# Optimization experiments

Measured on AMD Instinct MI355X. Metric: run time of the kernel, lower is better.

Reference implementation:

```python
import jax, jax.numpy as jnp
import numpy as np

B, S, H, I, NH, E = 16, 512, 1024, 4096, 16, 8
DH = H // NH
EPS = 1e-12


def layer_norm(x, g, b):
    mu = jnp.mean(x, axis=-1, keepdims=True)
    var = jnp.mean(jnp.square(x - mu), axis=-1, keepdims=True)
    return (x - mu) * jax.lax.rsqrt(var + EPS) * g + b


def setup_inputs() -> dict:
    key = jax.random.key(0)
    ks = jax.random.split(key, 16)
    s_h = 1.0 / np.sqrt(H)
    s_i = 1.0 / np.sqrt(I)
    return {
        "hidden_states": jax.random.normal(ks[0], (B, S, H), jnp.float32),
        "Wq": jax.random.normal(ks[1], (H, H), jnp.float32) * s_h,
        "bq": jnp.zeros((H,), jnp.float32),
        "Wk": jax.random.normal(ks[2], (H, H), jnp.float32) * s_h,
        "bk": jnp.zeros((H,), jnp.float32),
        "Wv": jax.random.normal(ks[3], (H, H), jnp.float32) * s_h,
        "bv": jnp.zeros((H,), jnp.float32),
        "Wo": jax.random.normal(ks[4], (H, H), jnp.float32) * s_h,
        "bo": jnp.zeros((H,), jnp.float32),
        "ln1_g": jnp.ones((H,), jnp.float32),
        "ln1_b": jnp.zeros((H,), jnp.float32),
        "ln2_g": jnp.ones((H,), jnp.float32),
        "ln2_b": jnp.zeros((H,), jnp.float32),
        "gate_W": jax.random.normal(ks[5], (H, E), jnp.float32) * s_h,
        "W_up": jax.random.normal(ks[6], (E, H, I), jnp.float32) * s_h,
        "b_up": jnp.zeros((E, I), jnp.float32),
        "W_down": jax.random.normal(ks[7], (E, I, H), jnp.float32) * s_i,
        "b_down": jnp.zeros((E, H), jnp.float32),
    }


def reference(hidden_states, Wq, bq, Wk, bk, Wv, bv, Wo, bo,
              ln1_g, ln1_b, ln2_g, ln2_b, gate_W, W_up, b_up, W_down, b_down):
    x = hidden_states
    # --- BERT self-attention ---
    q = (x @ Wq + bq).reshape(B, S, NH, DH)
    k = (x @ Wk + bk).reshape(B, S, NH, DH)
    v = (x @ Wv + bv).reshape(B, S, NH, DH)
    scores = jnp.einsum("bqhd,bkhd->bhqk", q, k) / np.sqrt(DH)
    probs = jax.nn.softmax(scores, axis=-1)
    ctx = jnp.einsum("bhqk,bkhd->bqhd", probs, v).reshape(B, S, H)
    # BertSelfOutput: dense + residual + LayerNorm
    attn_out = layer_norm(ctx @ Wo + bo + x, ln1_g, ln1_b)

    # --- feed_forward_chunk: pre-LN, MoE, residual (residual on attn_out) ---
    x_ln = layer_norm(attn_out, ln2_g, ln2_b)
    router_output = jnp.einsum("bsh,he->bse", x_ln, gate_W)
    router_logits = jnp.mean(router_output, axis=1)          # [B, E]
    choice = jnp.argmax(router_logits, axis=-1)              # softmax-argmax == logits-argmax

    # per-sample top-1 expert: gather each sample's expert weights, batched GEMM
    Wu = W_up[choice]                                        # [B, H, I]
    Wd = W_down[choice]                                      # [B, I, H]
    h = jax.nn.gelu(jnp.einsum("bsh,bhi->bsi", x_ln, Wu) + b_up[choice][:, None, :],
                    approximate=False)
    moe = jnp.einsum("bsi,bih->bsh", h, Wd) + b_down[choice][:, None, :]
    layer_output = moe + attn_out
    return (layer_output, router_logits)
```

## Files before the change

kernel.cpp:

```cpp
#include <hip/hip_runtime.h>


typedef __attribute__((ext_vector_type(4))) float f32x4;
typedef __attribute__((ext_vector_type(8))) short s8v;
typedef __attribute__((ext_vector_type(4))) short s4v;
typedef unsigned short u16;

#define DEV static __device__ __forceinline__

DEV u16 f2bf(float f){
  union { float f; unsigned u; } v; v.f = f;
  unsigned r = v.u + 0x7fffu + ((v.u >> 16) & 1u);
  return (u16)(r >> 16);
}

DEV f32x4 mfma16(s8v a, s8v b, f32x4 c){
  return __builtin_amdgcn_mfma_f32_16x16x32_bf16(a, b, c, 0, 0, 0);
}

DEV float wave_sum(float s){
#pragma unroll
  for (int o = 1; o < 64; o <<= 1) s += __shfl_xor(s, o);
  return s;
}

#define ASYNC_COPY16(g, l) \
  __builtin_amdgcn_global_load_lds((const __attribute__((address_space(1))) void*)(g), \
                                   (__attribute__((address_space(3))) void*)(l), 16, 0, 0)

__global__ __launch_bounds__(256) void cvt_bf16(const float* __restrict__ in,
                                                u16* __restrict__ out)
{
  const size_t i = ((size_t)blockIdx.x * 256 + threadIdx.x) * 8;
  f32x4 a = *(const f32x4*)&in[i];
  f32x4 b = *(const f32x4*)&in[i + 4];
  s8v o;
#pragma unroll
  for (int j = 0; j < 4; ++j){ o[j] = (short)f2bf(a[j]); o[4 + j] = (short)f2bf(b[j]); }
  *(s8v*)&out[i] = o;
}

__global__ __launch_bounds__(256) void transpose_w(const float* __restrict__ in,
                                                   u16* __restrict__ out, int R, int C)
{
  __shared__ float t[32][33];
  const size_t bs = (size_t)blockIdx.z * R * (size_t)C;
  in += bs; out += bs;
  const int c0 = blockIdx.x * 32, r0 = blockIdx.y * 32;
  const int tx = threadIdx.x & 31, ty = threadIdx.x >> 5;
#pragma unroll
  for (int j = 0; j < 32; j += 8) t[ty + j][tx] = in[(size_t)(r0 + ty + j) * C + c0 + tx];
  __syncthreads();
#pragma unroll
  for (int j = 0; j < 32; j += 8) out[(size_t)(c0 + ty + j) * R + r0 + tx] = f2bf(t[tx][ty + j]);
}

template<int MODE>
__global__ __launch_bounds__(256, 2) void gemm_bt(
    const u16* __restrict__ A, const u16* __restrict__ Bt,
    const float* __restrict__ bias, void* __restrict__ outp,
    const float* __restrict__ resid, int M, int N, int K,
    const int* __restrict__ choice,
    long aBatch, long outBatch, long residBatch, long btExpert, long biasExpert)
{
  const int z = blockIdx.z;
  if (choice){
    const int e = choice[z];
    Bt   += (size_t)e * btExpert;
    bias += (size_t)e * biasExpert;
  }
  A += (size_t)z * aBatch;

  const int tid = threadIdx.x;
  const int lane = tid & 63, wid = tid >> 6;
  const int hi = lane >> 4, l15 = lane & 15;
  const int wr = wid >> 1, wc = wid & 1;
  const long row0 = (long)blockIdx.x * 128;
  const long col0 = (long)blockIdx.y * 128;

  __shared__ __align__(16) u16 lA[128 * 32];
  __shared__ __align__(16) u16 lB[128 * 32];

  f32x4 acc[4][4];
#pragma unroll
  for (int i = 0; i < 4; ++i)
#pragma unroll
    for (int j = 0; j < 4; ++j) acc[i][j] = f32x4{0.f, 0.f, 0.f, 0.f};

  const int c1 = tid, c2 = tid + 256;
  const u16* sA1 = A  + (row0 + (c1 >> 2)) * (size_t)K + (c1 & 3) * 8;
  const u16* sA2 = A  + (row0 + (c2 >> 2)) * (size_t)K + (c2 & 3) * 8;
  const u16* sB1 = Bt + (col0 + (c1 >> 2)) * (size_t)K + (c1 & 3) * 8;
  const u16* sB2 = Bt + (col0 + (c2 >> 2)) * (size_t)K + (c2 & 3) * 8;
  u16* dA1 = &lA[c1 * 8]; u16* dA2 = &lA[c2 * 8];
  u16* dB1 = &lB[c1 * 8]; u16* dB2 = &lB[c2 * 8];

  for (int kt = 0; kt < K; kt += 32){
    ASYNC_COPY16(sA1, dA1);
    ASYNC_COPY16(sA2, dA2);
    ASYNC_COPY16(sB1, dB1);
    ASYNC_COPY16(sB2, dB2);
    sA1 += 32; sA2 += 32; sB1 += 32; sB2 += 32;
    asm volatile("s_waitcnt vmcnt(0)" ::: "memory");
    __syncthreads();

    s8v af[4], bf[4];
#pragma unroll
    for (int mi = 0; mi < 4; ++mi)
      af[mi] = *(const s8v*)&lA[(wr * 64 + mi * 16 + l15) * 32 + hi * 8];
#pragma unroll
    for (int ni = 0; ni < 4; ++ni)
      bf[ni] = *(const s8v*)&lB[(wc * 64 + ni * 16 + l15) * 32 + hi * 8];
#pragma unroll
    for (int mi = 0; mi < 4; ++mi)
#pragma unroll
      for (int ni = 0; ni < 4; ++ni)
        acc[mi][ni] = mfma16(af[mi], bf[ni], acc[mi][ni]);
    __syncthreads();
  }

#pragma unroll
  for (int mi = 0; mi < 4; ++mi){
    const long rowb = row0 + wr * 64 + mi * 16 + hi * 4;
#pragma unroll
    for (int ni = 0; ni < 4; ++ni){
      const long col = col0 + wc * 64 + ni * 16 + l15;
      const float bv = bias[col];
#pragma unroll
      for (int r = 0; r < 4; ++r){
        const long row = rowb + r;
        float v = acc[mi][ni][r] + bv;
        if (MODE == 2){
          float* o = (float*)outp + (size_t)z * outBatch;
          const float* rs = resid + (size_t)z * residBatch;
          o[row * N + col] = v + rs[row * N + col];
        } else if (MODE == 0){
          u16* o = (u16*)outp + (size_t)z * outBatch;
          o[row * N + col] = f2bf(v);
        } else if (MODE == 1){
          u16* o = (u16*)outp + (size_t)z * outBatch;
          const float gv = 0.5f * v * (1.0f + erff(v * 0.70710678118654752f));
          o[row * N + col] = f2bf(gv);
        } else {
          const int bb = (int)(row >> 9), ss = (int)(row & 511);
          const int hh = (int)(col >> 6), dd = (int)(col & 63);
          ((u16*)outp)[(((size_t)(bb * 16 + hh)) * 64 + dd) * 512 + ss] = f2bf(v);
        }
      }
    }
  }
}

__global__ __launch_bounds__(256, 2) void attn_fwd(
    const u16* __restrict__ qb, const u16* __restrict__ kb,
    const u16* __restrict__ vt, u16* __restrict__ ctx)
{
  const int lane = threadIdx.x & 63, wid = threadIdx.x >> 6;
  const int hi = lane >> 4, l15 = lane & 15;
  const int h = blockIdx.y, b = blockIdx.z;
  const int q0 = blockIdx.x * 64 + wid * 16;

  const u16* qp  = qb + ((size_t)b * 512 + q0) * 1024 + h * 64;
  const u16* kp0 = kb + (size_t)b * 512 * 1024 + h * 64;
  const u16* vp  = vt + ((size_t)(b * 16 + h)) * 64 * 512;

  __shared__ __align__(16) u16 P[4][16][40];

  const s8v qf0 = *(const s8v*)&qp[(size_t)l15 * 1024 + hi * 8];
  const s8v qf1 = *(const s8v*)&qp[(size_t)l15 * 1024 + 32 + hi * 8];

  f32x4 o[4];
#pragma unroll
  for (int mi = 0; mi < 4; ++mi) o[mi] = f32x4{0.f, 0.f, 0.f, 0.f};
  float mrun = -3e38f, lrun = 0.f;

  for (int k0 = 0; k0 < 512; k0 += 32){
    const u16* kp = kp0 + (size_t)k0 * 1024;
    f32x4 s0 = f32x4{0.f,0.f,0.f,0.f}, s1 = f32x4{0.f,0.f,0.f,0.f};
    s0 = mfma16(*(const s8v*)&kp[(size_t)l15 * 1024 + hi * 8],             qf0, s0);
    s0 = mfma16(*(const s8v*)&kp[(size_t)l15 * 1024 + 32 + hi * 8],        qf1, s0);
    s1 = mfma16(*(const s8v*)&kp[(size_t)(16 + l15) * 1024 + hi * 8],      qf0, s1);
    s1 = mfma16(*(const s8v*)&kp[(size_t)(16 + l15) * 1024 + 32 + hi * 8], qf1, s1);

    float mx = fmaxf(fmaxf(fmaxf(s0[0], s0[1]), fmaxf(s0[2], s0[3])),
                     fmaxf(fmaxf(s1[0], s1[1]), fmaxf(s1[2], s1[3]))) * 0.125f;
    mx = fmaxf(mx, __shfl_xor(mx, 16));
    mx = fmaxf(mx, __shfl_xor(mx, 32));
    const float mnew = fmaxf(mrun, mx);
    const float alpha = __expf(mrun - mnew);
    mrun = mnew;

    float p[8]; float ps = 0.f;
#pragma unroll
    for (int r = 0; r < 4; ++r){ p[r]     = __expf(s0[r] * 0.125f - mnew); ps += p[r]; }
#pragma unroll
    for (int r = 0; r < 4; ++r){ p[4 + r] = __expf(s1[r] * 0.125f - mnew); ps += p[4 + r]; }
    ps += __shfl_xor(ps, 16);
    ps += __shfl_xor(ps, 32);
    lrun = lrun * alpha + ps;
#pragma unroll
    for (int mi = 0; mi < 4; ++mi)
#pragma unroll
      for (int r = 0; r < 4; ++r) o[mi][r] *= alpha;

    s4v pk0, pk1;
#pragma unroll
    for (int r = 0; r < 4; ++r){ pk0[r] = (short)f2bf(p[r]); pk1[r] = (short)f2bf(p[4 + r]); }
    *(s4v*)&P[wid][l15][4 * hi]      = pk0;
    *(s4v*)&P[wid][l15][16 + 4 * hi] = pk1;

    const s8v pf = *(const s8v*)&P[wid][l15][8 * hi];
#pragma unroll
    for (int mi = 0; mi < 4; ++mi)
      o[mi] = mfma16(*(const s8v*)&vp[(size_t)(mi * 16 + l15) * 512 + k0 + 8 * hi], pf, o[mi]);
  }

  const float inv = 1.f / lrun;
  u16* cp = ctx + ((size_t)b * 512 + q0 + l15) * 1024 + h * 64;
#pragma unroll
  for (int mi = 0; mi < 4; ++mi)
#pragma unroll
    for (int r = 0; r < 4; ++r)
      cp[mi * 16 + 4 * hi + r] = f2bf(o[mi][r] * inv);
}

__global__ __launch_bounds__(256, 2) void ln_inplace(float* __restrict__ x,
    const float* __restrict__ g, const float* __restrict__ be)
{
  const int row = blockIdx.x * 4 + (threadIdx.x >> 6);
  const int lane = threadIdx.x & 63;
  float* p = x + (size_t)row * 1024;
  f32x4 v[4];
#pragma unroll
  for (int c = 0; c < 4; ++c) v[c] = *(const f32x4*)&p[c * 256 + lane * 4];
  float s = 0.f;
#pragma unroll
  for (int c = 0; c < 4; ++c){ s += v[c][0] + v[c][1] + v[c][2] + v[c][3]; }
  const float mu = wave_sum(s) * (1.f / 1024.f);
  float s2 = 0.f;
#pragma unroll
  for (int c = 0; c < 4; ++c)
#pragma unroll
    for (int j = 0; j < 4; ++j){ const float d = v[c][j] - mu; s2 += d * d; }
  const float rs = rsqrtf(wave_sum(s2) * (1.f / 1024.f) + 1e-12f);
#pragma unroll
  for (int c = 0; c < 4; ++c){
    const f32x4 gg = *(const f32x4*)&g[c * 256 + lane * 4];
    const f32x4 bb = *(const f32x4*)&be[c * 256 + lane * 4];
    f32x4 ov;
#pragma unroll
    for (int j = 0; j < 4; ++j) ov[j] = (v[c][j] - mu) * rs * gg[j] + bb[j];
    *(f32x4*)&p[c * 256 + lane * 4] = ov;
  }
}

__global__ __launch_bounds__(256, 2) void ln2_colsum(
    const float* __restrict__ attn, const float* __restrict__ g, const float* __restrict__ be,
    u16* __restrict__ xln, float* __restrict__ colsum)
{
  const int b = blockIdx.y;
  const int wid = threadIdx.x >> 6, lane = threadIdx.x & 63;
  __shared__ float cacc[1024];
  for (int i = threadIdx.x; i < 1024; i += 256) cacc[i] = 0.f;
  __syncthreads();
  float acc[16];
#pragma unroll
  for (int i = 0; i < 16; ++i) acc[i] = 0.f;
  const int rbase = b * 512 + blockIdx.x * 64 + wid * 16;
  for (int rr = 0; rr < 16; ++rr){
    const float* p = attn + (size_t)(rbase + rr) * 1024;
    f32x4 v[4];
#pragma unroll
    for (int c = 0; c < 4; ++c) v[c] = *(const f32x4*)&p[c * 256 + lane * 4];
    float s = 0.f;
#pragma unroll
    for (int c = 0; c < 4; ++c) s += v[c][0] + v[c][1] + v[c][2] + v[c][3];
    const float mu = wave_sum(s) * (1.f / 1024.f);
    float s2 = 0.f;
#pragma unroll
    for (int c = 0; c < 4; ++c)
#pragma unroll
      for (int j = 0; j < 4; ++j){ const float d = v[c][j] - mu; s2 += d * d; }
    const float rs = rsqrtf(wave_sum(s2) * (1.f / 1024.f) + 1e-12f);
    u16* op = xln + (size_t)(rbase + rr) * 1024;
#pragma unroll
    for (int c = 0; c < 4; ++c){
      const f32x4 gg = *(const f32x4*)&g[c * 256 + lane * 4];
      const f32x4 bb = *(const f32x4*)&be[c * 256 + lane * 4];
      s4v ov;
#pragma unroll
      for (int j = 0; j < 4; ++j){
        const float y = (v[c][j] - mu) * rs * gg[j] + bb[j];
        acc[c * 4 + j] += y;
        ov[j] = (short)f2bf(y);
      }
      *(s4v*)&op[c * 256 + lane * 4] = ov;
    }
  }
#pragma unroll
  for (int c = 0; c < 4; ++c)
#pragma unroll
    for (int j = 0; j < 4; ++j)
      atomicAdd(&cacc[c * 256 + lane * 4 + j], acc[c * 4 + j]);
  __syncthreads();
  for (int i = threadIdx.x; i < 1024; i += 256) atomicAdd(&colsum[b * 1024 + i], cacc[i]);
}

__global__ void router_argmax(const float* __restrict__ colsum, const float* __restrict__ gate,
                              float* __restrict__ logits, int* __restrict__ choice)
{
  const int b = blockIdx.x, lane = threadIdx.x;
  float pa[8];
#pragma unroll
  for (int e = 0; e < 8; ++e) pa[e] = 0.f;
  for (int it = 0; it < 16; ++it){
    const int hh = it * 64 + lane;
    const float c = colsum[b * 1024 + hh];
    const float* gp = gate + (size_t)hh * 8;
#pragma unroll
    for (int e = 0; e < 8; ++e) pa[e] += c * gp[e];
  }
#pragma unroll
  for (int e = 0; e < 8; ++e) pa[e] = wave_sum(pa[e]);
  if (lane == 0){
    float best = -3e38f; int bi = 0;
#pragma unroll
    for (int e = 0; e < 8; ++e){
      const float lg = pa[e] * (1.f / 512.f);
      logits[b * 8 + e] = lg;
      if (lg > best){ best = lg; bi = e; }
    }
    choice[b] = bi;
  }
}

extern "C" void kernel_launch(void* const* d_in, const int* in_sizes, int n_in,
                              void* d_out, int out_size, void* d_ws, size_t ws_size,
                              hipStream_t stream)
{
  const float* x    = (const float*)d_in[0];
  const float* Wq   = (const float*)d_in[1];
  const float* bq   = (const float*)d_in[2];
  const float* Wk   = (const float*)d_in[3];
  const float* bk   = (const float*)d_in[4];
  const float* Wv   = (const float*)d_in[5];
  const float* bv   = (const float*)d_in[6];
  const float* Wo   = (const float*)d_in[7];
  const float* bo   = (const float*)d_in[8];
  const float* ln1g = (const float*)d_in[9];
  const float* ln1b = (const float*)d_in[10];
  const float* ln2g = (const float*)d_in[11];
  const float* ln2b = (const float*)d_in[12];
  const float* gate = (const float*)d_in[13];
  const float* Wup  = (const float*)d_in[14];
  const float* bup  = (const float*)d_in[15];
  const float* Wdn  = (const float*)d_in[16];
  const float* bdn  = (const float*)d_in[17];

  size_t off = 0;
  char* wsb = (char*)d_ws;
  auto take = [&](size_t n) -> void* {
    void* p = wsb + off; off += (n + 255) & ~(size_t)255; return p;
  };
  u16*   x_bf  = (u16*)take(8192ull * 1024 * 2);
  u16*   Wqt   = (u16*)take(1024ull * 1024 * 2);
  u16*   Wkt   = (u16*)take(1024ull * 1024 * 2);
  u16*   Wvt   = (u16*)take(1024ull * 1024 * 2);
  u16*   Wot   = (u16*)take(1024ull * 1024 * 2);
  u16*   q_bf  = (u16*)take(8192ull * 1024 * 2);
  u16*   k_bf  = (u16*)take(8192ull * 1024 * 2);
  u16*   vt_bf = (u16*)take(8192ull * 1024 * 2);
  float* tmp   = (float*)take(8192ull * 1024 * 4);
  u16*   Wupt  = (u16*)take(8ull * 4096 * 1024 * 2);
  u16*   Wdnt  = (u16*)take(8ull * 1024 * 4096 * 2);
  u16*   h_bf  = (u16*)take(8192ull * 4096 * 2);
  float* colsum = (float*)take(16ull * 1024 * 4);
  int*   choice = (int*)take(256);

  u16* ctx = x_bf;
  u16* xln = q_bf;
  float* logits = (float*)d_out + 8388608;

  cvt_bf16<<<4096, 256, 0, stream>>>(x, x_bf);
  transpose_w<<<dim3(32, 32, 1),  256, 0, stream>>>(Wq,  Wqt,  1024, 1024);
  transpose_w<<<dim3(32, 32, 1),  256, 0, stream>>>(Wk,  Wkt,  1024, 1024);
  transpose_w<<<dim3(32, 32, 1),  256, 0, stream>>>(Wv,  Wvt,  1024, 1024);
  transpose_w<<<dim3(32, 32, 1),  256, 0, stream>>>(Wo,  Wot,  1024, 1024);
  transpose_w<<<dim3(128, 32, 8), 256, 0, stream>>>(Wup, Wupt, 1024, 4096);
  transpose_w<<<dim3(32, 128, 8), 256, 0, stream>>>(Wdn, Wdnt, 4096, 1024);

  gemm_bt<0><<<dim3(64, 8, 1), 256, 0, stream>>>(x_bf, Wqt, bq, q_bf,  nullptr,
      8192, 1024, 1024, nullptr, 0, 0, 0, 0, 0);
  gemm_bt<0><<<dim3(64, 8, 1), 256, 0, stream>>>(x_bf, Wkt, bk, k_bf,  nullptr,
      8192, 1024, 1024, nullptr, 0, 0, 0, 0, 0);
  gemm_bt<3><<<dim3(64, 8, 1), 256, 0, stream>>>(x_bf, Wvt, bv, vt_bf, nullptr,
      8192, 1024, 1024, nullptr, 0, 0, 0, 0, 0);

  attn_fwd<<<dim3(8, 16, 16), 256, 0, stream>>>(q_bf, k_bf, vt_bf, ctx);

  gemm_bt<2><<<dim3(64, 8, 1), 256, 0, stream>>>(ctx, Wot, bo, tmp, x,
      8192, 1024, 1024, nullptr, 0, 0, 0, 0, 0);
  ln_inplace<<<2048, 256, 0, stream>>>(tmp, ln1g, ln1b);

  hipMemsetAsync(colsum, 0, 16 * 1024 * sizeof(float), stream);
  ln2_colsum<<<dim3(8, 16), 256, 0, stream>>>(tmp, ln2g, ln2b, xln, colsum);
  router_argmax<<<16, 64, 0, stream>>>(colsum, gate, logits, choice);

  gemm_bt<1><<<dim3(4, 32, 16), 256, 0, stream>>>(xln, Wupt, bup, h_bf, nullptr,
      512, 4096, 1024, choice, 512ll * 1024, 512ll * 4096, 0, 4096ll * 1024, 4096);
  gemm_bt<2><<<dim3(4, 8, 16), 256, 0, stream>>>(h_bf, Wdnt, bdn, d_out, tmp,
      512, 1024, 4096, choice, 512ll * 4096, 512ll * 1024, 512ll * 1024, 1024ll * 4096, 1024);
}
```

Baseline: 628.7 us.

## Stage K/V tiles in LDS with double-buffered async copies in attention

The attention kernel now copies 64-key K and V tiles into swizzled LDS using async global-to-LDS copies with double buffering. Each wave handles 32 queries instead of 16, so every staged tile is reused across more queries. This replaces per-wave direct global loads of K and V with shared, overlapped loads. The transpose kernel also moves from 32x32 to 64x64 tiles. The larger LDS footprint and more registers per wave may lower occupancy.

```diff
diff --git a/kernel.cpp b/kernel.cpp
--- a/kernel.cpp
+++ b/kernel.cpp
@@ -43,16 +43,16 @@
 __global__ __launch_bounds__(256) void transpose_w(const float* __restrict__ in,
                                                    u16* __restrict__ out, int R, int C)
 {
-  __shared__ float t[32][33];
+  __shared__ float t[64][65];
   const size_t bs = (size_t)blockIdx.z * R * (size_t)C;
   in += bs; out += bs;
-  const int c0 = blockIdx.x * 32, r0 = blockIdx.y * 32;
-  const int tx = threadIdx.x & 31, ty = threadIdx.x >> 5;
-#pragma unroll
-  for (int j = 0; j < 32; j += 8) t[ty + j][tx] = in[(size_t)(r0 + ty + j) * C + c0 + tx];
+  const int c0 = blockIdx.x * 64, r0 = blockIdx.y * 64;
+  const int tx = threadIdx.x & 63, ty = threadIdx.x >> 6;
+#pragma unroll
+  for (int j = 0; j < 64; j += 4) t[ty + j][tx] = in[(size_t)(r0 + ty + j) * C + c0 + tx];
   __syncthreads();
 #pragma unroll
-  for (int j = 0; j < 32; j += 8) out[(size_t)(c0 + ty + j) * R + r0 + tx] = f2bf(t[tx][ty + j]);
+  for (int j = 0; j < 64; j += 4) out[(size_t)(c0 + ty + j) * R + r0 + tx] = f2bf(t[tx][ty + j]);
 }
 
 template<int MODE>
@@ -151,77 +151,139 @@
   }
 }
 
-__global__ __launch_bounds__(256, 2) void attn_fwd(
+__global__ __launch_bounds__(256) void attn_fwd(
     const u16* __restrict__ qb, const u16* __restrict__ kb,
     const u16* __restrict__ vt, u16* __restrict__ ctx)
 {
-  const int lane = threadIdx.x & 63, wid = threadIdx.x >> 6;
+  const int tid = threadIdx.x;
+  const int lane = tid & 63, wid = tid >> 6;
   const int hi = lane >> 4, l15 = lane & 15;
   const int h = blockIdx.y, b = blockIdx.z;
-  const int q0 = blockIdx.x * 64 + wid * 16;
-
-  const u16* qp  = qb + ((size_t)b * 512 + q0) * 1024 + h * 64;
+  const int q0 = blockIdx.x * 128 + wid * 32;
+
   const u16* kp0 = kb + (size_t)b * 512 * 1024 + h * 64;
-  const u16* vp  = vt + ((size_t)(b * 16 + h)) * 64 * 512;
-
-  __shared__ __align__(16) u16 P[4][16][40];
-
-  const s8v qf0 = *(const s8v*)&qp[(size_t)l15 * 1024 + hi * 8];
-  const s8v qf1 = *(const s8v*)&qp[(size_t)l15 * 1024 + 32 + hi * 8];
-
-  f32x4 o[4];
-#pragma unroll
-  for (int mi = 0; mi < 4; ++mi) o[mi] = f32x4{0.f, 0.f, 0.f, 0.f};
-  float mrun = -3e38f, lrun = 0.f;
-
-  for (int k0 = 0; k0 < 512; k0 += 32){
-    const u16* kp = kp0 + (size_t)k0 * 1024;
-    f32x4 s0 = f32x4{0.f,0.f,0.f,0.f}, s1 = f32x4{0.f,0.f,0.f,0.f};
-    s0 = mfma16(*(const s8v*)&kp[(size_t)l15 * 1024 + hi * 8],             qf0, s0);
-    s0 = mfma16(*(const s8v*)&kp[(size_t)l15 * 1024 + 32 + hi * 8],        qf1, s0);
-    s1 = mfma16(*(const s8v*)&kp[(size_t)(16 + l15) * 1024 + hi * 8],      qf0, s1);
-    s1 = mfma16(*(const s8v*)&kp[(size_t)(16 + l15) * 1024 + 32 + hi * 8], qf1, s1);
-
-    float mx = fmaxf(fmaxf(fmaxf(s0[0], s0[1]), fmaxf(s0[2], s0[3])),
-                     fmaxf(fmaxf(s1[0], s1[1]), fmaxf(s1[2], s1[3]))) * 0.125f;
-    mx = fmaxf(mx, __shfl_xor(mx, 16));
-    mx = fmaxf(mx, __shfl_xor(mx, 32));
-    const float mnew = fmaxf(mrun, mx);
-    const float alpha = __expf(mrun - mnew);
-    mrun = mnew;
-
-    float p[8]; float ps = 0.f;
-#pragma unroll
-    for (int r = 0; r < 4; ++r){ p[r]     = __expf(s0[r] * 0.125f - mnew); ps += p[r]; }
-#pragma unroll
-    for (int r = 0; r < 4; ++r){ p[4 + r] = __expf(s1[r] * 0.125f - mnew); ps += p[4 + r]; }
-    ps += __shfl_xor(ps, 16);
-    ps += __shfl_xor(ps, 32);
-    lrun = lrun * alpha + ps;
+  const u16* vp0 = vt + ((size_t)(b * 16 + h)) * 64 * 512;
+
+  __shared__ __align__(16) u16 lK[2][64 * 64];
+  __shared__ __align__(16) u16 lV[2][64 * 64];
+  __shared__ __align__(16) u16 lP[4][2][16][72];
+
+#define STAGE(bsel, k0s) do { \
+  _Pragma("unroll") \
+  for (int i = 0; i < 2; ++i){ \
+    const int idx = i * 256 + tid; \
+    const int row = idx >> 3, seg = idx & 7; \
+    const int sc = ((seg ^ (row & 7)) << 3); \
+    ASYNC_COPY16(kp0 + (size_t)((k0s) + row) * 1024 + sc, &lK[bsel][idx * 8]); \
+    ASYNC_COPY16(vp0 + (size_t)row * 512 + (k0s) + sc,    &lV[bsel][idx * 8]); \
+  } \
+} while (0)
+
+  const u16* qp = qb + ((size_t)b * 512 + q0) * 1024 + h * 64;
+  s8v qf[2][2];
+#pragma unroll
+  for (int qt = 0; qt < 2; ++qt)
+#pragma unroll
+    for (int st = 0; st < 2; ++st)
+      qf[qt][st] = *(const s8v*)&qp[(size_t)(qt * 16 + l15) * 1024 + st * 32 + hi * 8];
+
+  f32x4 o[2][4];
+#pragma unroll
+  for (int qt = 0; qt < 2; ++qt)
+#pragma unroll
+    for (int mi = 0; mi < 4; ++mi) o[qt][mi] = f32x4{0.f, 0.f, 0.f, 0.f};
+  float mrun[2] = {-3e38f, -3e38f}, lrun[2] = {0.f, 0.f};
+
+  STAGE(0, 0);
+  __syncthreads();
+
+  for (int t = 0; t < 8; ++t){
+    const int buf = t & 1;
+    if (t < 7) STAGE(buf ^ 1, (t + 1) * 64);
+
+    f32x4 s[2][4];
+#pragma unroll
+    for (int qt = 0; qt < 2; ++qt)
+#pragma unroll
+      for (int kt = 0; kt < 4; ++kt) s[qt][kt] = f32x4{0.f, 0.f, 0.f, 0.f};
+#pragma unroll
+    for (int st = 0; st < 2; ++st){
+      s8v kf[4];
+#pragma unroll
+      for (int kt = 0; kt < 4; ++kt){
+        const int row = kt * 16 + l15;
+        kf[kt] = *(const s8v*)&lK[buf][row * 64 + (((st * 4 + hi) ^ (row & 7)) << 3)];
+      }
+#pragma unroll
+      for (int qt = 0; qt < 2; ++qt)
+#pragma unroll
+        for (int kt = 0; kt < 4; ++kt)
+          s[qt][kt] = mfma16(kf[kt], qf[qt][st], s[qt][kt]);
+    }
+
+#pragma unroll
+    for (int qt = 0; qt < 2; ++qt){
+      float mx = s[qt][0][0];
+#pragma unroll
+      for (int kt = 0; kt < 4; ++kt)
+#pragma unroll
+        for (int r = 0; r < 4; ++r) mx = fmaxf(mx, s[qt][kt][r]);
+      mx *= 0.125f;
+      mx = fmaxf(mx, __shfl_xor(mx, 16));
+      mx = fmaxf(mx, __shfl_xor(mx, 32));
+      const float mnew = fmaxf(mrun[qt], mx);
+      const float alpha = __expf(mrun[qt] - mnew);
+      mrun[qt] = mnew;
+      float ps = 0.f;
+#pragma unroll
+      for (int kt = 0; kt < 4; ++kt){
+        s4v pk;
+#pragma unroll
+        for (int r = 0; r < 4; ++r){
+          const float p = __expf(s[qt][kt][r] * 0.125f - mnew);
+          ps += p; pk[r] = (short)f2bf(p);
+        }
+        *(s4v*)&lP[wid][qt][l15][kt * 16 + 4 * hi] = pk;
+      }
+      ps += __shfl_xor(ps, 16);
+      ps += __shfl_xor(ps, 32);
+      lrun[qt] = lrun[qt] * alpha + ps;
+#pragma unroll
+      for (int mi = 0; mi < 4; ++mi)
+#pragma unroll
+        for (int r = 0; r < 4; ++r) o[qt][mi][r] *= alpha;
+    }
+
+#pragma unroll
+    for (int ks = 0; ks < 2; ++ks){
+      s8v vf[4];
+#pragma unroll
+      for (int mi = 0; mi < 4; ++mi){
+        const int row = mi * 16 + l15;
+        vf[mi] = *(const s8v*)&lV[buf][row * 64 + (((ks * 4 + hi) ^ (row & 7)) << 3)];
+      }
+#pragma unroll
+      for (int qt = 0; qt < 2; ++qt){
+        const s8v pf = *(const s8v*)&lP[wid][qt][l15][ks * 32 + 8 * hi];
+#pragma unroll
+        for (int mi = 0; mi < 4; ++mi)
+          o[qt][mi] = mfma16(vf[mi], pf, o[qt][mi]);
+      }
+    }
+    __syncthreads();
+  }
+#undef STAGE
+
+#pragma unroll
+  for (int qt = 0; qt < 2; ++qt){
+    const float inv = 1.f / lrun[qt];
+    u16* cp = ctx + ((size_t)b * 512 + q0 + qt * 16 + l15) * 1024 + h * 64;
 #pragma unroll
     for (int mi = 0; mi < 4; ++mi)
 #pragma unroll
-      for (int r = 0; r < 4; ++r) o[mi][r] *= alpha;
-
-    s4v pk0, pk1;
-#pragma unroll
-    for (int r = 0; r < 4; ++r){ pk0[r] = (short)f2bf(p[r]); pk1[r] = (short)f2bf(p[4 + r]); }
-    *(s4v*)&P[wid][l15][4 * hi]      = pk0;
-    *(s4v*)&P[wid][l15][16 + 4 * hi] = pk1;
-
-    const s8v pf = *(const s8v*)&P[wid][l15][8 * hi];
-#pragma unroll
-    for (int mi = 0; mi < 4; ++mi)
-      o[mi] = mfma16(*(const s8v*)&vp[(size_t)(mi * 16 + l15) * 512 + k0 + 8 * hi], pf, o[mi]);
-  }
-
-  const float inv = 1.f / lrun;
-  u16* cp = ctx + ((size_t)b * 512 + q0 + l15) * 1024 + h * 64;
-#pragma unroll
-  for (int mi = 0; mi < 4; ++mi)
-#pragma unroll
-    for (int r = 0; r < 4; ++r)
-      cp[mi * 16 + 4 * hi + r] = f2bf(o[mi][r] * inv);
+      for (int r = 0; r < 4; ++r)
+        cp[mi * 16 + 4 * hi + r] = f2bf(o[qt][mi][r] * inv);
+  }
 }
 
 __global__ __launch_bounds__(256, 2) void ln_inplace(float* __restrict__ x,
@@ -382,12 +444,12 @@
   float* logits = (float*)d_out + 8388608;
 
   cvt_bf16<<<4096, 256, 0, stream>>>(x, x_bf);
-  transpose_w<<<dim3(32, 32, 1),  256, 0, stream>>>(Wq,  Wqt,  1024, 1024);
-  transpose_w<<<dim3(32, 32, 1),  256, 0, stream>>>(Wk,  Wkt,  1024, 1024);
-  transpose_w<<<dim3(32, 32, 1),  256, 0, stream>>>(Wv,  Wvt,  1024, 1024);
-  transpose_w<<<dim3(32, 32, 1),  256, 0, stream>>>(Wo,  Wot,  1024, 1024);
-  transpose_w<<<dim3(128, 32, 8), 256, 0, stream>>>(Wup, Wupt, 1024, 4096);
-  transpose_w<<<dim3(32, 128, 8), 256, 0, stream>>>(Wdn, Wdnt, 4096, 1024);
+  transpose_w<<<dim3(16, 16, 1), 256, 0, stream>>>(Wq,  Wqt,  1024, 1024);
+  transpose_w<<<dim3(16, 16, 1), 256, 0, stream>>>(Wk,  Wkt,  1024, 1024);
+  transpose_w<<<dim3(16, 16, 1), 256, 0, stream>>>(Wv,  Wvt,  1024, 1024);
+  transpose_w<<<dim3(16, 16, 1), 256, 0, stream>>>(Wo,  Wot,  1024, 1024);
+  transpose_w<<<dim3(64, 16, 8), 256, 0, stream>>>(Wup, Wupt, 1024, 4096);
+  transpose_w<<<dim3(16, 64, 8), 256, 0, stream>>>(Wdn, Wdnt, 4096, 1024);
 
   gemm_bt<0><<<dim3(64, 8, 1), 256, 0, stream>>>(x_bf, Wqt, bq, q_bf,  nullptr,
       8192, 1024, 1024, nullptr, 0, 0, 0, 0, 0);
@@ -396,7 +458,7 @@
   gemm_bt<3><<<dim3(64, 8, 1), 256, 0, stream>>>(x_bf, Wvt, bv, vt_bf, nullptr,
       8192, 1024, 1024, nullptr, 0, 0, 0, 0, 0);
 
-  attn_fwd<<<dim3(8, 16, 16), 256, 0, stream>>>(q_bf, k_bf, vt_bf, ctx);
+  attn_fwd<<<dim3(4, 16, 16), 256, 0, stream>>>(q_bf, k_bf, vt_bf, ctx);
 
   gemm_bt<2><<<dim3(64, 8, 1), 256, 0, stream>>>(ctx, Wot, bo, tmp, x,
       8192, 1024, 1024, nullptr, 0, 0, 0, 0, 0);
```

Measured after the change: 552.7 us. 12.1% less time.
